# Kernel optimization log

Measured on AMD Instinct MI355X. Metric: run time of the kernel, lower is better.

## Reference

```python
import jax, jax.numpy as jnp
from jax import lax
import numpy as np

BN_EPS = 1e-5  # nn.BatchNorm2d default eps (eval mode with running stats)


def setup_inputs() -> dict:
    key = jax.random.key(0)
    ks = jax.random.split(key, 6)
    B, C, O, H, W = 4, 64, 64, 128, 128
    x = jax.random.normal(ks[0], (B, C, H, W), jnp.float32)
    # conv_offset: 27 = 3 * deform_groups * kh * kw output channels, zero-bias.
    # Scaled small to mimic the near-zero init of ModulatedDeformConv2dPack.
    w_off = jax.random.normal(ks[1], (27, C, 3, 3), jnp.float32) * 0.05
    b_off = jnp.zeros((27,), jnp.float32)
    weight = jax.random.normal(ks[2], (O, C, 3, 3), jnp.float32) * (1.0 / np.sqrt(C * 9))
    bias = jax.random.normal(ks[3], (O,), jnp.float32) * 0.1
    gamma = jax.random.normal(ks[4], (O,), jnp.float32) * 0.1 + 1.0
    beta = jax.random.normal(ks[5], (O,), jnp.float32) * 0.1
    running_mean = jnp.zeros((O,), jnp.float32)
    running_var = jnp.ones((O,), jnp.float32)
    return {"x": x, "w_off": w_off, "b_off": b_off, "weight": weight, "bias": bias,
            "gamma": gamma, "beta": beta, "running_mean": running_mean, "running_var": running_var}


def _dcn_bn_relu(x, w_off, b_off, weight, bias, gamma, beta, running_mean, running_var):
    B, C, H, W = x.shape
    O = weight.shape[0]
    K = 9  # 3x3 kernel taps
    # --- offset/mask conv (regular 3x3, stride 1, pad 1) ---
    off = lax.conv_general_dilated(x, w_off, (1, 1), ((1, 1), (1, 1)),
                                   dimension_numbers=("NCHW", "OIHW", "NCHW"))
    off = off + b_off[None, :, None, None]
    o1, o2, m = jnp.split(off, 3, axis=1)  # each [B,9,H,W]
    # mmcv layout: cat(o1,o2) then interpreted as (tap, [y,x]) pairs
    offset = jnp.concatenate([o1, o2], axis=1).reshape(B, K, 2, H, W)
    mask = jax.nn.sigmoid(m)  # [B,K,H,W]
    # --- sampling grid: p = (h - pad + i*dil + dy, w - pad + j*dil + dx) ---
    ky = (jnp.repeat(jnp.arange(3), 3) - 1).astype(x.dtype)  # [K]
    kx = (jnp.tile(jnp.arange(3), 3) - 1).astype(x.dtype)
    py = jnp.arange(H, dtype=x.dtype)[None, None, :, None] + ky[None, :, None, None] + offset[:, :, 0]
    px = jnp.arange(W, dtype=x.dtype)[None, None, None, :] + kx[None, :, None, None] + offset[:, :, 1]
    y0 = jnp.floor(py); x0 = jnp.floor(px)
    dy = py - y0; dx = px - x0  # [B,K,H,W]
    y0i = y0.astype(jnp.int32); x0i = x0.astype(jnp.int32)

    def gather(yi, xi):
        # zero outside bounds (mmcv bilinear semantics)
        valid = (yi >= 0) & (yi < H) & (xi >= 0) & (xi < W)
        yc = jnp.clip(yi, 0, H - 1)
        xc = jnp.clip(xi, 0, W - 1)
        g = jax.vmap(lambda xb, yb, xb2: xb[:, yb, xb2])(x, yc, xc)  # [B,C,K,H,W]
        return g * valid[:, None].astype(x.dtype)

    w00 = ((1 - dy) * (1 - dx))[:, None]
    w01 = ((1 - dy) * dx)[:, None]
    w10 = (dy * (1 - dx))[:, None]
    w11 = (dy * dx)[:, None]
    samp = (gather(y0i, x0i) * w00 + gather(y0i, x0i + 1) * w01 +
            gather(y0i + 1, x0i) * w10 + gather(y0i + 1, x0i + 1) * w11)
    samp = samp * mask[:, None]  # modulation, [B,C,K,H,W]
    # conv accumulation over (channel, tap)
    out = jnp.einsum("ock,bckhw->bohw", weight.reshape(O, C, K), samp)
    out = out + bias[None, :, None, None]
    # --- BatchNorm2d (eval, running stats) + ReLU ---
    scale = gamma / jnp.sqrt(running_var + BN_EPS)
    out = (out - running_mean[None, :, None, None]) * scale[None, :, None, None] + beta[None, :, None, None]
    return jax.nn.relu(out)


def reference(x, w_off, b_off, weight, bias, gamma, beta, running_mean, running_var):
    return _dcn_bn_relu(x, w_off, b_off, weight, bias, gamma, beta, running_mean, running_var)
```

## Files before the change

kernel.cpp:

```cpp
#include <hip/hip_runtime.h>
#include <hip/hip_bf16.h>


#define HH 128
#define WW 128
#define KP2 200

typedef __attribute__((ext_vector_type(8))) short bf16x8;
typedef __attribute__((ext_vector_type(4))) float f32x4;

__device__ __forceinline__ unsigned short f2bf(float f) {
    union { __hip_bfloat16 b; unsigned short u; } cv;
    cv.b = __float2bfloat16(f);
    return cv.u;
}
__device__ __forceinline__ float bf2f(unsigned short u) {
    union { unsigned int i; float f; } cv;
    cv.i = ((unsigned int)u) << 16;
    return cv.f;
}
__device__ __forceinline__ unsigned int cvt_pk_bf16(float a, float b) {
    unsigned int r;
    asm("v_cvt_pk_bf16_f32 %0, %1, %2" : "=v"(r) : "v"(a), "v"(b));
    return r;
}

#define WBM_ELEMS 36864
#define WBO_ELEMS 18432
#define XT_OFF    55296

__global__ __launch_bounds__(256) void transpose_kernel(
    const float* __restrict__ x,
    const float* __restrict__ w_off,
    const float* __restrict__ wgt,
    unsigned short* __restrict__ ws)
{
    __shared__ float tile[64 * 65];
    const int tid = threadIdx.x;

    {
        int t = blockIdx.x * 256 + tid;
        if (t < WBM_ELEMS) {
            int j = t & 7, lane = (t >> 3) & 63, nt = (t >> 9) & 3, kb = t >> 11;
            int k = kb * 32 + ((lane >> 4) << 3) + j;
            int n = nt * 16 + (lane & 15);
            int tap = k >> 6, c = k & 63;
            ws[t] = f2bf(wgt[n * 576 + c * 9 + tap]);
        } else if (t < WBM_ELEMS + WBO_ELEMS) {
            int t2 = t - WBM_ELEMS;
            int j = t2 & 7, lane = (t2 >> 3) & 63, nt = (t2 >> 9) & 1, kb = t2 >> 10;
            int k = kb * 32 + ((lane >> 4) << 3) + j;
            int n = nt * 16 + (lane & 15);
            int tap = k >> 6, c = k & 63;
            ws[t] = (n < 27) ? f2bf(w_off[n * 576 + c * 9 + tap]) : (unsigned short)0;
        }
    }

    const int bb  = blockIdx.x >> 8;
    const int hw0 = (blockIdx.x & 255) << 6;
    const float* xb = x + ((size_t)bb << 20);
#pragma unroll
    for (int it = 0; it < 16; ++it) {
        int idx = it * 256 + tid;
        int c = idx >> 6, i = idx & 63;
        tile[c * 65 + i] = xb[(c << 14) + hw0 + i];
    }
    __syncthreads();
    unsigned int* xtb = (unsigned int*)(ws + XT_OFF) + ((size_t)bb << 19);
#pragma unroll
    for (int it = 0; it < 8; ++it) {
        int idx = it * 256 + tid;
        int i = idx >> 5, c2 = idx & 31;
        xtb[(size_t)(hw0 + i) * 32 + c2] =
            cvt_pk_bf16(tile[(2 * c2) * 65 + i], tile[(2 * c2 + 1) * 65 + i]);
    }
}

__global__ __launch_bounds__(256, 8) void DeformConv_14568529068723_kernel(
    const float* __restrict__ b_off,
    const float* __restrict__ bias,
    const float* __restrict__ gamma,
    const float* __restrict__ beta,
    const float* __restrict__ rmean,
    const float* __restrict__ rvar,
    const unsigned short* __restrict__ ws,
    float* __restrict__ out)
{
    __shared__ __align__(16) unsigned short samp[32 * KP2];
    __shared__ __align__(16) float eL[4][9][32];
    __shared__ int   oL[2][9][32];
    __shared__ float sbuf[176];

    const int tid  = threadIdx.x;
    const int wv   = tid >> 6;
    const int lane = tid & 63;
    const int px16 = lane & 15;
    const int cg   = lane >> 4;
    const int c8   = tid & 7;
    const int pxq  = tid >> 3;

    if (tid < 64) {
        float sc = gamma[tid] * __frsqrt_rn(rvar[tid] + 1e-5f);
        sbuf[tid] = sc;
        sbuf[64 + tid] = (bias[tid] - rmean[tid]) * sc + beta[tid];
        if (tid < 27) sbuf[128 + tid] = b_off[tid];
    }

    const int bid = blockIdx.x;
    const int swz = ((bid & 7) << 8) + (bid >> 3);
    const int p0   = swz * 32;
    const int b    = p0 >> 14;
    const int rem0 = p0 & 16383;
    const int h    = rem0 >> 7;
    const int w0   = rem0 & 127;
    const unsigned short* xt = ws + XT_OFF + ((size_t)b << 20);

    const bf16x8* WbM = (const bf16x8*)ws;
    const bf16x8* WbO = (const bf16x8*)(ws + WBM_ELEMS);

    unsigned short* rbrow2 = (unsigned short*)eL;

    for (int i = tid; i < 816; i += 256) {
        int j = i / 272;
        int rem = i - j * 272;
        int cc = rem >> 3, c8i = rem & 7;
        int yy = h + j - 1;
        int gx = w0 - 1 + cc;
        bool ok = (yy >= 0) & (yy < HH) & (gx >= 0) & (gx < WW);
        int pos = min(max(yy, 0), HH - 1) * WW + min(max(gx, 0), WW - 1);
        uint4 v = *(const uint4*)(xt + pos * 64 + (c8i << 3));
        if (!ok) { v.x = 0u; v.y = 0u; v.z = 0u; v.w = 0u; }
        unsigned short* rb = (j < 2) ? &samp[j * 2176] : rbrow2;
        *(uint4*)&rb[cc * 64 + ((c8i ^ (cc & 7)) << 3)] = v;
    }
    __syncthreads();

    f32x4 accO[2];
#pragma unroll
    for (int q = 0; q < 2; ++q) accO[q] = (f32x4){0.f, 0.f, 0.f, 0.f};

    if (wv < 2) {
        __builtin_amdgcn_s_setprio(1);
#pragma unroll
        for (int chk = 0; chk < 3; ++chk) {
            const unsigned short* rb = (chk < 2) ? &samp[chk * 2176]
                                                 : (const unsigned short*)rbrow2;
#pragma unroll
            for (int st = 0; st < 6; ++st) {
                int kb = chk * 6 + st;
                int tl = st >> 1;
                int g0 = (st & 1) * 4 + cg;
                bf16x8 bO = WbO[(kb * 2 + wv) * 64 + lane];
#pragma unroll
                for (int mt = 0; mt < 2; ++mt) {
                    int col = mt * 16 + px16 + tl;
                    bf16x8 af = *(const bf16x8*)&rb[(col * 64) + (((g0 ^ (col & 7)) << 3))];
                    accO[mt] = __builtin_amdgcn_mfma_f32_16x16x32_bf16(af, bO, accO[mt], 0, 0, 0);
                }
            }
        }
        __builtin_amdgcn_s_setprio(0);
    }
    __syncthreads();

    float* offs = (float*)samp;
    if (wv < 2) {
        int n0 = wv * 16 + (lane & 15);
        int mB = cg * 4;
        if (n0 < 27) {
#pragma unroll
            for (int mt = 0; mt < 2; ++mt)
#pragma unroll
                for (int r = 0; r < 4; ++r) {
                    int pxc = mt * 16 + mB + r;
                    float vv = accO[mt][r] + sbuf[128 + n0];
                    if (n0 >= 18) vv = 1.0f / (1.0f + __expf(-vv));
                    offs[n0 * 32 + pxc] = vv;
                }
        }
    }
    __syncthreads();

#pragma unroll
    for (int base = 0; base < 288; base += 256) {
        int idx = base + tid;
        if (idx < 288) {
            int px = idx & 31, tap = idx >> 5;
            float o1 = offs[(2 * tap) * 32 + px];
            float o2 = offs[(2 * tap + 1) * 32 + px];
            float m  = offs[(18 + tap) * 32 + px];
            float py  = (float)(h + tap / 3 - 1) + o1;
            float pxf = (float)(w0 + px + tap % 3 - 1) + o2;
            float y0f = floorf(py), x0f = floorf(pxf);
            float dy = py - y0f, dx = pxf - x0f;
            int y0 = (int)y0f, x0 = (int)x0f;
            int y1 = y0 + 1, x1 = x0 + 1;
            int yc0 = min(max(y0, 0), HH - 1), yc1 = min(max(y1, 0), HH - 1);
            int xc0 = min(max(x0, 0), WW - 1), xc1 = min(max(x1, 0), WW - 1);
            float vy0 = (y0 >= 0 && y0 < HH) ? 1.0f : 0.0f;
            float vy1 = (y1 >= 0 && y1 < HH) ? 1.0f : 0.0f;
            float vx0 = (x0 >= 0 && x0 < WW) ? 1.0f : 0.0f;
            float vx1 = (x1 >= 0 && x1 < WW) ? 1.0f : 0.0f;
            float c00 = (1.0f - dy) * (1.0f - dx) * m * vy0 * vx0;
            float c01 = (1.0f - dy) * dx * m * vy0 * vx1;
            float c10 = dy * (1.0f - dx) * m * vy1 * vx0;
            float c11 = dy * dx * m * vy1 * vx1;
            int bx = min(xc0, WW - 2);
            bool s0 = (xc0 != bx), s1 = (xc1 != bx);
            eL[0][tap][px] = (s0 ? 0.f : c00) + (s1 ? 0.f : c01);
            eL[1][tap][px] = (s0 ? c00 : 0.f) + (s1 ? c01 : 0.f);
            eL[2][tap][px] = (s0 ? 0.f : c10) + (s1 ? 0.f : c11);
            eL[3][tap][px] = (s0 ? c10 : 0.f) + (s1 ? c11 : 0.f);
            oL[0][tap][px] = (yc0 * WW + bx) * 64;
            oL[1][tap][px] = (yc1 * WW + bx) * 64;
        }
    }
    __syncthreads();

    f32x4 acc[2];
#pragma unroll
    for (int mt = 0; mt < 2; ++mt) acc[mt] = (f32x4){0.f, 0.f, 0.f, 0.f};

    for (int chk = 0; chk < 3; ++chk) {
#pragma unroll
        for (int tl = 0; tl < 3; ++tl) {
            int tap = chk * 3 + tl;
            int o0 = oL[0][tap][pxq], o1r = oL[1][tap][pxq];
            float e0 = eL[0][tap][pxq], e1 = eL[1][tap][pxq];
            float e2 = eL[2][tap][pxq], e3 = eL[3][tap][pxq];
            uint4 a0 = *(const uint4*)(xt + o0 + (c8 << 3));
            uint4 a1 = *(const uint4*)(xt + o0 + 64 + (c8 << 3));
            uint4 b0 = *(const uint4*)(xt + o1r + (c8 << 3));
            uint4 b1 = *(const uint4*)(xt + o1r + 64 + (c8 << 3));
            const unsigned int* pa0 = (const unsigned int*)&a0;
            const unsigned int* pa1 = (const unsigned int*)&a1;
            const unsigned int* pb0 = (const unsigned int*)&b0;
            const unsigned int* pb1 = (const unsigned int*)&b1;
            uint4 pk;
            unsigned int* pp = (unsigned int*)&pk;
#pragma unroll
            for (int q = 0; q < 4; ++q) {
                float lo = e0 * bf2f((unsigned short)(pa0[q] & 0xffff))
                         + e1 * bf2f((unsigned short)(pa1[q] & 0xffff))
                         + e2 * bf2f((unsigned short)(pb0[q] & 0xffff))
                         + e3 * bf2f((unsigned short)(pb1[q] & 0xffff));
                float hi = e0 * bf2f((unsigned short)(pa0[q] >> 16))
                         + e1 * bf2f((unsigned short)(pa1[q] >> 16))
                         + e2 * bf2f((unsigned short)(pb0[q] >> 16))
                         + e3 * bf2f((unsigned short)(pb1[q] >> 16));
                pp[q] = cvt_pk_bf16(lo, hi);
            }
            *(uint4*)&samp[pxq * KP2 + tl * 64 + (c8 << 3)] = pk;
        }
        __syncthreads();
        __builtin_amdgcn_s_setprio(1);
#pragma unroll
        for (int st = 0; st < 6; ++st) {
            int kb = chk * 6 + st;
            bf16x8 bf = WbM[(kb * 4 + wv) * 64 + lane];
            bf16x8 af0 = *(const bf16x8*)&samp[px16 * KP2 + st * 32 + (cg << 3)];
            bf16x8 af1 = *(const bf16x8*)&samp[(16 + px16) * KP2 + st * 32 + (cg << 3)];
            acc[0] = __builtin_amdgcn_mfma_f32_16x16x32_bf16(af0, bf, acc[0], 0, 0, 0);
            acc[1] = __builtin_amdgcn_mfma_f32_16x16x32_bf16(af1, bf, acc[1], 0, 0, 0);
        }
        __builtin_amdgcn_s_setprio(0);
        __syncthreads();
    }

    float* dT = (float*)samp;
    {
        int n0 = lane & 15;
        int mB = cg * 4;
#pragma unroll
        for (int mt = 0; mt < 2; ++mt)
#pragma unroll
            for (int r = 0; r < 4; ++r)
                dT[(wv * 16 + n0) * 33 + mt * 16 + mB + r] = acc[mt][r];
    }
    __syncthreads();
    {
        int px = tid & 31;
        int oh = tid >> 5;
#pragma unroll
        for (int i = 0; i < 8; ++i) {
            int o = 8 * i + oh;
            float v = dT[o * 33 + px];
            v = fmaxf(fmaf(v, sbuf[o], sbuf[64 + o]), 0.0f);
            out[(((size_t)(b * 64 + o)) << 14) + rem0 + px] = v;
        }
    }
}

extern "C" void kernel_launch(void* const* d_in, const int* in_sizes, int n_in,
                              void* d_out, int out_size, void* d_ws, size_t ws_size,
                              hipStream_t stream) {
    (void)in_sizes; (void)n_in; (void)ws_size; (void)out_size;
    const float* x     = (const float*)d_in[0];
    const float* w_off = (const float*)d_in[1];
    const float* b_off = (const float*)d_in[2];
    const float* wgt   = (const float*)d_in[3];
    const float* bias  = (const float*)d_in[4];
    const float* gamma = (const float*)d_in[5];
    const float* beta  = (const float*)d_in[6];
    const float* rmean = (const float*)d_in[7];
    const float* rvar  = (const float*)d_in[8];
    unsigned short* wsB = (unsigned short*)d_ws;
    float* outp = (float*)d_out;

    transpose_kernel<<<dim3(1024), dim3(256), 0, stream>>>(x, w_off, wgt, wsB);
    DeformConv_14568529068723_kernel<<<dim3(2048), dim3(256), 0, stream>>>(
        b_off, bias, gamma, beta, rmean, rvar, wsB, outp);
}
```

Baseline: 108.1 us.

## Spread offset-conv MFMA across all four waves and store output directly from accumulators

The offset/mask convolution MFMA work, previously done by two waves with two tiles each, is split so each of the four waves computes one 16x16 tile. This removes idle waves and shortens the critical path. The epilogue drops the LDS transpose and its extra barriers: each lane applies BN+ReLU to its accumulator and writes four contiguous floats per tile straight to global memory. The last loop barrier is also skipped. The trade-off is less-coalesced global stores, 16-byte chunks strided across channels rather than full 128-byte rows.

New measurement: 109.9 us. About the same (+1.7%).

```diff
diff --git a/kernel.cpp b/kernel.cpp
--- a/kernel.cpp
+++ b/kernel.cpp
@@ -135,11 +135,11 @@
     }
     __syncthreads();
 
-    f32x4 accO[2];
-#pragma unroll
-    for (int q = 0; q < 2; ++q) accO[q] = (f32x4){0.f, 0.f, 0.f, 0.f};
-
-    if (wv < 2) {
+    const int ocO = wv & 1;
+    const int mtO = wv >> 1;
+    f32x4 accO = (f32x4){0.f, 0.f, 0.f, 0.f};
+
+    {
         __builtin_amdgcn_s_setprio(1);
 #pragma unroll
         for (int chk = 0; chk < 3; ++chk) {
@@ -150,13 +150,10 @@
                 int kb = chk * 6 + st;
                 int tl = st >> 1;
                 int g0 = (st & 1) * 4 + cg;
-                bf16x8 bO = WbO[(kb * 2 + wv) * 64 + lane];
-#pragma unroll
-                for (int mt = 0; mt < 2; ++mt) {
-                    int col = mt * 16 + px16 + tl;
-                    bf16x8 af = *(const bf16x8*)&rb[(col * 64) + (((g0 ^ (col & 7)) << 3))];
-                    accO[mt] = __builtin_amdgcn_mfma_f32_16x16x32_bf16(af, bO, accO[mt], 0, 0, 0);
-                }
+                bf16x8 bO = WbO[(kb * 2 + ocO) * 64 + lane];
+                int col = mtO * 16 + px16 + tl;
+                bf16x8 af = *(const bf16x8*)&rb[(col * 64) + (((g0 ^ (col & 7)) << 3))];
+                accO = __builtin_amdgcn_mfma_f32_16x16x32_bf16(af, bO, accO, 0, 0, 0);
             }
         }
         __builtin_amdgcn_s_setprio(0);
@@ -164,19 +161,18 @@
     __syncthreads();
 
     float* offs = (float*)samp;
-    if (wv < 2) {
-        int n0 = wv * 16 + (lane & 15);
+    {
+        int n0 = ocO * 16 + (lane & 15);
         int mB = cg * 4;
         if (n0 < 27) {
-#pragma unroll
-            for (int mt = 0; mt < 2; ++mt)
-#pragma unroll
-                for (int r = 0; r < 4; ++r) {
-                    int pxc = mt * 16 + mB + r;
-                    float vv = accO[mt][r] + sbuf[128 + n0];
-                    if (n0 >= 18) vv = 1.0f / (1.0f + __expf(-vv));
-                    offs[n0 * 32 + pxc] = vv;
-                }
+            float bo = sbuf[128 + n0];
+#pragma unroll
+            for (int r = 0; r < 4; ++r) {
+                int pxc = mtO * 16 + mB + r;
+                float vv = accO[r] + bo;
+                if (n0 >= 18) vv = 1.0f / (1.0f + __expf(-vv));
+                offs[n0 * 32 + pxc] = vv;
+            }
         }
     }
     __syncthreads();
@@ -264,29 +260,20 @@
             acc[1] = __builtin_amdgcn_mfma_f32_16x16x32_bf16(af1, bf, acc[1], 0, 0, 0);
         }
         __builtin_amdgcn_s_setprio(0);
-        __syncthreads();
-    }
-
-    float* dT = (float*)samp;
+        if (chk < 2) __syncthreads();
+    }
+
     {
-        int n0 = lane & 15;
-        int mB = cg * 4;
-#pragma unroll
-        for (int mt = 0; mt < 2; ++mt)
+        int o = wv * 16 + (lane & 15);
+        float sc = sbuf[o], b2 = sbuf[64 + o];
+        float* op = out + (((size_t)(b * 64 + o)) << 14) + rem0;
+#pragma unroll
+        for (int mt = 0; mt < 2; ++mt) {
+            f32x4 st;
 #pragma unroll
             for (int r = 0; r < 4; ++r)
-                dT[(wv * 16 + n0) * 33 + mt * 16 + mB + r] = acc[mt][r];
-    }
-    __syncthreads();
-    {
-        int px = tid & 31;
-        int oh = tid >> 5;
-#pragma unroll
-        for (int i = 0; i < 8; ++i) {
-            int o = 8 * i + oh;
-            float v = dT[o * 33 + px];
-            v = fmaxf(fmaf(v, sbuf[o], sbuf[64 + o]), 0.0f);
-            out[(((size_t)(b * 64 + o)) << 14) + rem0 + px] = v;
+                st[r] = fmaxf(fmaf(acc[mt][r], sc, b2), 0.0f);
+            *(f32x4*)(op + mt * 16 + cg * 4) = st;
         }
     }
 }
```
